# Optimization experiments

Measured on AMD Instinct MI355X. Metric: run time of the kernel, lower is better.

The kernel has to match this reference:

```python
import jax, jax.numpy as jnp
import numpy as np

IN_CH = 63      # positionally-encoded points
IN_VIEWS = 63   # positionally-encoded view dirs (must equal IN_CH per source bug)
UNITS = 256
N = 131072
SKIPS = (4,)


def _linear_init(key, fan_in, fan_out):
    # torch nn.Linear default: U(-1/sqrt(fan_in), 1/sqrt(fan_in)) for W and b
    kw, kb = jax.random.split(key)
    bound = 1.0 / np.sqrt(fan_in)
    W = jax.random.uniform(kw, (fan_in, fan_out), jnp.float32, -bound, bound)
    b = jax.random.uniform(kb, (fan_out,), jnp.float32, -bound, bound)
    return W, b


def setup_inputs() -> dict:
    key = jax.random.key(0)
    keys = jax.random.split(key, 16)
    inp = {}
    inp["x"] = jax.random.normal(keys[0], (N, IN_CH + IN_VIEWS), jnp.float32)
    # 8 backbone layers; layer idx 5 consumes skip-concat of width UNITS+IN_CH
    fan_ins = [IN_CH] + [UNITS + IN_CH if (i - 1) in SKIPS else UNITS for i in range(1, 8)]
    for i, fi in enumerate(fan_ins):
        W, b = _linear_init(keys[1 + i], fi, UNITS)
        inp[f"W{i}"], inp[f"b{i}"] = W, b
    inp["Wf"], inp["bf"] = _linear_init(keys[9], UNITS, UNITS)          # linear_feature
    inp["Wa"], inp["ba"] = _linear_init(keys[10], UNITS, 1)             # linear_alpha
    inp["Wv"], inp["bv"] = _linear_init(keys[11], IN_CH + UNITS, UNITS // 2)  # linear_views[0]
    inp["Wr"], inp["br"] = _linear_init(keys[12], UNITS // 2, 3)        # linear_rgb
    return inp


def reference(x, W0, b0, W1, b1, W2, b2, W3, b3, W4, b4, W5, b5, W6, b6, W7, b7,
              Wf, bf, Wa, ba, Wv, bv, Wr, br):
    pts = x[..., :IN_CH]
    views = x[..., IN_CH:]
    Ws = (W0, W1, W2, W3, W4, W5, W6, W7)
    bs = (b0, b1, b2, b3, b4, b5, b6, b7)
    h = pts
    for idx in range(8):
        h = jax.nn.relu(h @ Ws[idx] + bs[idx])
        if idx in SKIPS:
            h = jnp.concatenate([pts, h], axis=-1)  # [N, IN_CH + UNITS]
    alpha = h @ Wa + ba                       # [N, 1]
    feature = h @ Wf + bf                     # [N, UNITS]
    hv = jnp.concatenate([feature, views], axis=-1)   # [N, UNITS + IN_VIEWS]
    hv = jax.nn.relu(hv @ Wv + bv)            # [N, UNITS//2]
    rgb = hv @ Wr + br                        # [N, 3]
    return jnp.concatenate([rgb, alpha], axis=-1)     # [N, 4]
```

## Files before the change

kernel.cpp:

```cpp
#include <hip/hip_runtime.h>
#include <hip/hip_bf16.h>


typedef __bf16 bfrag __attribute__((ext_vector_type(8)));
typedef float  f4    __attribute__((ext_vector_type(4)));

constexpr int OFF_W0 = 0;
constexpr int OFF_W1 = 16384;
constexpr int OFF_W2 = 81920;
constexpr int OFF_W3 = 147456;
constexpr int OFF_W4 = 212992;
constexpr int OFF_W5 = 278528;
constexpr int OFF_W6 = 360448;
constexpr int OFF_W7 = 425984;
constexpr int OFF_WF = 491520;
constexpr int OFF_WV = 557056;
constexpr int OFF_WA = 598016;
constexpr int OFF_WR = 602112;
constexpr int WS_TOTAL = 604160;

__device__ __forceinline__ unsigned swz256(int row, int k) {
  return (unsigned)((row * 256 + k) ^ ((row & 7) << 3));
}
__device__ __forceinline__ unsigned swz64(int row, int k) {
  return (unsigned)((row * 64 + k) ^ ((row & 7) << 3));
}

template<int NCT, int NKS, int NCTS, int SSTR>
__device__ __forceinline__ void phase(f4 (&acc)[4][NCT],
    const unsigned short* __restrict__ src,
    const unsigned short* __restrict__ wt, int ks0, int ctb,
    int lane, int l15, int lk8) {
#pragma unroll
  for (int ks = 0; ks < NKS; ++ks) {
    const int kl = ks * 32 + lk8;
    bfrag a[4];
#pragma unroll
    for (int rt = 0; rt < 4; ++rt) {
      const unsigned idx = (SSTR == 256) ? swz256(rt * 16 + l15, kl)
                                         : swz64(rt * 16 + l15, kl);
      a[rt] = *(const bfrag*)(src + idx);
    }
    const unsigned short* wk =
        wt + ((size_t)(ks0 + ks) * NCTS + ctb) * 512 + lane * 8;
    constexpr int CH = (NCT < 2) ? NCT : 2;
#pragma unroll
    for (int c2 = 0; c2 < NCT; c2 += CH) {
      bfrag b[CH];
#pragma unroll
      for (int u = 0; u < CH; ++u)
        b[u] = *(const bfrag*)(wk + (size_t)(c2 + u) * 512);
#pragma unroll
      for (int u = 0; u < CH; ++u)
#pragma unroll
        for (int rt = 0; rt < 4; ++rt)
          acc[rt][c2 + u] = __builtin_amdgcn_mfma_f32_16x16x32_bf16(a[rt], b[u], acc[rt][c2 + u], 0, 0, 0);
    }
  }
}

template<int NCT>
__device__ __forceinline__ void init_acc(f4 (&acc)[4][NCT],
    const float* __restrict__ bias, int cb, int l15) {
#pragma unroll
  for (int ct = 0; ct < NCT; ++ct) {
    const float bv = bias[cb + ct * 16 + l15];
    f4 v = {bv, bv, bv, bv};
#pragma unroll
    for (int rt = 0; rt < 4; ++rt) acc[rt][ct] = v;
  }
}

template<bool RELU, int NCT>
__device__ __forceinline__ void store_h(f4 (&acc)[4][NCT],
    unsigned short* __restrict__ h, int cb, int l15, int lk4) {
#pragma unroll
  for (int ct = 0; ct < NCT; ++ct) {
    const int col = cb + ct * 16 + l15;
#pragma unroll
    for (int rt = 0; rt < 4; ++rt)
#pragma unroll
      for (int j = 0; j < 4; ++j) {
        float v = acc[rt][ct][j];
        if (RELU) v = fmaxf(v, 0.f);
        __bf16 bb = (__bf16)v;
        h[swz256(rt * 16 + lk4 + j, col)] = __builtin_bit_cast(unsigned short, bb);
      }
  }
}

__device__ __forceinline__ void stage_inputs(const float* __restrict__ x,
    unsigned short* pts, unsigned short* views, int rowg0, int tid) {
  const int row = tid >> 2, seg = tid & 3;
  const float* xr = x + (size_t)(rowg0 + row) * 126;
  bfrag v0, v1;
#pragma unroll
  for (int q = 0; q < 4; ++q) {
    const int c = seg * 16 + 2 * q;
    float2 t = *(const float2*)(xr + c);
    v0[2 * q]     = (c     < 63) ? (__bf16)t.x : (__bf16)0.f;
    v0[2 * q + 1] = (c + 1 < 63) ? (__bf16)t.y : (__bf16)0.f;
  }
#pragma unroll
  for (int q = 0; q < 4; ++q) {
    const int c = seg * 16 + 8 + 2 * q;
    float2 t = *(const float2*)(xr + c);
    v1[2 * q]     = (c     < 63) ? (__bf16)t.x : (__bf16)0.f;
    v1[2 * q + 1] = (c + 1 < 63) ? (__bf16)t.y : (__bf16)0.f;
  }
  *(bfrag*)(pts + swz64(row, seg * 16))     = v0;
  *(bfrag*)(pts + swz64(row, seg * 16 + 8)) = v1;
  bfrag w0, w1;
#pragma unroll
  for (int j = 0; j < 8; ++j) {
    const int c = seg * 16 + j;
    w0[j] = (c < 63) ? (__bf16)xr[63 + c] : (__bf16)0.f;
  }
#pragma unroll
  for (int j = 0; j < 8; ++j) {
    const int c = seg * 16 + 8 + j;
    w1[j] = (c < 63) ? (__bf16)xr[63 + c] : (__bf16)0.f;
  }
  *(bfrag*)(views + swz64(row, seg * 16))     = w0;
  *(bfrag*)(views + swz64(row, seg * 16 + 8)) = w1;
}

struct RepackArgs {
  const float *W0, *W1, *W2, *W3, *W4, *W5, *W6, *W7, *Wf, *Wv, *Wa, *Wr;
  unsigned short* ws;
};

__global__ void repack_kernel(RepackArgs a) {
  const int i = blockIdx.x * 256 + threadIdx.x;
  if (i >= WS_TOTAL) return;

  const float* src; int off, ncts, fanin, fanout; bool shift = false;
  int mode = 0;
  if      (i < OFF_W1) { src = a.W0; off = OFF_W0; ncts = 16; fanin = 63;  fanout = 256; }
  else if (i < OFF_W2) { src = a.W1; off = OFF_W1; ncts = 16; fanin = 256; fanout = 256; }
  else if (i < OFF_W3) { src = a.W2; off = OFF_W2; ncts = 16; fanin = 256; fanout = 256; }
  else if (i < OFF_W4) { src = a.W3; off = OFF_W3; ncts = 16; fanin = 256; fanout = 256; }
  else if (i < OFF_W5) { src = a.W4; off = OFF_W4; ncts = 16; fanin = 256; fanout = 256; }
  else if (i < OFF_W6) { src = a.W5; off = OFF_W5; ncts = 16; fanin = 319; fanout = 256; shift = true; }
  else if (i < OFF_W7) { src = a.W6; off = OFF_W6; ncts = 16; fanin = 256; fanout = 256; }
  else if (i < OFF_WF) { src = a.W7; off = OFF_W7; ncts = 16; fanin = 256; fanout = 256; }
  else if (i < OFF_WV) { src = a.Wf; off = OFF_WF; ncts = 16; fanin = 256; fanout = 256; }
  else if (i < OFF_WA) { src = a.Wv; off = OFF_WV; ncts = 8;  fanin = 319; fanout = 128; }
  else if (i < OFF_WR) { src = a.Wa; off = OFF_WA; ncts = 1;  fanin = 256; fanout = 1; mode = 1; }
  else                 { src = a.Wr; off = OFF_WR; ncts = 1;  fanin = 128; fanout = 3; mode = 2; }

  const int idx  = i - off;
  const int j    = idx & 7;
  const int lane = (idx >> 3) & 63;
  const int rem  = idx >> 9;
  const int ctg  = rem % ncts;
  const int ks   = rem / ncts;
  const int k    = ks * 32 + ((lane >> 4) << 3) + j;
  const int col  = ctg * 16 + (lane & 15);

  float v;
  if (mode == 1) {
    v = (col == 0 && k < fanin) ? src[k] : 0.f;
  } else if (mode == 2) {
    v = (col < 3 && k < fanin) ? src[(size_t)k * 3 + col] : 0.f;
  } else if (shift) {
    v = (k < 63) ? src[(size_t)k * 256 + col]
                 : ((k == 63) ? 0.f : src[(size_t)(k - 1) * 256 + col]);
  } else {
    v = (k < fanin) ? src[(size_t)k * fanout + col] : 0.f;
  }
  __bf16 bb = (__bf16)v;
  a.ws[i] = __builtin_bit_cast(unsigned short, bb);
}

struct MainArgs {
  const float* x;
  const unsigned short* ws;
  const float *b0, *b1, *b2, *b3, *b4, *b5, *b6, *b7;
  const float *bfc, *ba, *bv, *br;
  float* out;
};

__global__ __launch_bounds__(256, 2) void nerf_kernel(MainArgs A) {
  extern __shared__ unsigned short lds[];
  unsigned short* h     = lds;
  unsigned short* pts   = lds + 64 * 256;
  unsigned short* views = pts + 64 * 64;

  const int tid  = threadIdx.x;
  const int lane = tid & 63;
  const int wave = tid >> 6;
  const int l15 = lane & 15;
  const int lk8 = (lane >> 4) << 3;
  const int lk4 = (lane >> 4) << 2;
  const int cb  = wave * 64;
  const int ctb = wave * 4;
  const int rowg0 = blockIdx.x * 64;
  const unsigned short* ws = A.ws;

  stage_inputs(A.x, pts, views, rowg0, tid);
  __syncthreads();

  f4 acc[4][4];

  init_acc<4>(acc, A.b0, cb, l15);
  phase<4, 2, 16, 64>(acc, pts, ws + OFF_W0, 0, ctb, lane, l15, lk8);
  store_h<true, 4>(acc, h, cb, l15, lk4);
  __syncthreads();

  init_acc<4>(acc, A.b1, cb, l15);
  phase<4, 8, 16, 256>(acc, h, ws + OFF_W1, 0, ctb, lane, l15, lk8);
  __syncthreads();
  store_h<true, 4>(acc, h, cb, l15, lk4);
  __syncthreads();

  init_acc<4>(acc, A.b2, cb, l15);
  phase<4, 8, 16, 256>(acc, h, ws + OFF_W2, 0, ctb, lane, l15, lk8);
  __syncthreads();
  store_h<true, 4>(acc, h, cb, l15, lk4);
  __syncthreads();

  init_acc<4>(acc, A.b3, cb, l15);
  phase<4, 8, 16, 256>(acc, h, ws + OFF_W3, 0, ctb, lane, l15, lk8);
  __syncthreads();
  store_h<true, 4>(acc, h, cb, l15, lk4);
  __syncthreads();

  init_acc<4>(acc, A.b4, cb, l15);
  phase<4, 8, 16, 256>(acc, h, ws + OFF_W4, 0, ctb, lane, l15, lk8);
  __syncthreads();
  store_h<true, 4>(acc, h, cb, l15, lk4);
  __syncthreads();

  init_acc<4>(acc, A.b5, cb, l15);
  phase<4, 2, 16, 64>(acc, pts, ws + OFF_W5, 0, ctb, lane, l15, lk8);
  phase<4, 8, 16, 256>(acc, h, ws + OFF_W5, 2, ctb, lane, l15, lk8);
  __syncthreads();
  store_h<true, 4>(acc, h, cb, l15, lk4);
  __syncthreads();

  init_acc<4>(acc, A.b6, cb, l15);
  phase<4, 8, 16, 256>(acc, h, ws + OFF_W6, 0, ctb, lane, l15, lk8);
  __syncthreads();
  store_h<true, 4>(acc, h, cb, l15, lk4);
  __syncthreads();

  init_acc<4>(acc, A.b7, cb, l15);
  phase<4, 8, 16, 256>(acc, h, ws + OFF_W7, 0, ctb, lane, l15, lk8);
  __syncthreads();
  store_h<true, 4>(acc, h, cb, l15, lk4);
  __syncthreads();

  if (wave == 0) {
    f4 accA[4][1];
#pragma unroll
    for (int rt = 0; rt < 4; ++rt) accA[rt][0] = (f4){0.f, 0.f, 0.f, 0.f};
    phase<1, 8, 1, 256>(accA, h, ws + OFF_WA, 0, 0, lane, l15, lk8);
    if (l15 == 0) {
      const float ba0 = A.ba[0];
#pragma unroll
      for (int rt = 0; rt < 4; ++rt)
#pragma unroll
        for (int j = 0; j < 4; ++j)
          A.out[(size_t)(rowg0 + rt * 16 + lk4 + j) * 4 + 3] = accA[rt][0][j] + ba0;
    }
  }

  init_acc<4>(acc, A.bfc, cb, l15);
  phase<4, 8, 16, 256>(acc, h, ws + OFF_WF, 0, ctb, lane, l15, lk8);
  __syncthreads();
  store_h<false, 4>(acc, h, cb, l15, lk4);
  __syncthreads();

  {
    f4 acc2[4][2];
    const int cb2 = wave * 32;
    init_acc<2>(acc2, A.bv, cb2, l15);
    phase<2, 8, 8, 256>(acc2, h, ws + OFF_WV, 0, wave * 2, lane, l15, lk8);
    phase<2, 2, 8, 64>(acc2, views, ws + OFF_WV, 8, wave * 2, lane, l15, lk8);
    __syncthreads();
    store_h<true, 2>(acc2, h, cb2, l15, lk4);
  }
  __syncthreads();

  if (wave == 0) {
    f4 accR[4][1];
#pragma unroll
    for (int rt = 0; rt < 4; ++rt) accR[rt][0] = (f4){0.f, 0.f, 0.f, 0.f};
    phase<1, 4, 1, 256>(accR, h, ws + OFF_WR, 0, 0, lane, l15, lk8);
    if (l15 < 3) {
      const float bb = A.br[l15];
#pragma unroll
      for (int rt = 0; rt < 4; ++rt)
#pragma unroll
        for (int j = 0; j < 4; ++j)
          A.out[(size_t)(rowg0 + rt * 16 + lk4 + j) * 4 + l15] = accR[rt][0][j] + bb;
    }
  }
}

extern "C" void kernel_launch(void* const* d_in, const int* in_sizes, int n_in,
                              void* d_out, int out_size, void* d_ws, size_t ws_size,
                              hipStream_t stream) {
  RepackArgs ra;
  ra.W0 = (const float*)d_in[1];  ra.W1 = (const float*)d_in[3];
  ra.W2 = (const float*)d_in[5];  ra.W3 = (const float*)d_in[7];
  ra.W4 = (const float*)d_in[9];  ra.W5 = (const float*)d_in[11];
  ra.W6 = (const float*)d_in[13]; ra.W7 = (const float*)d_in[15];
  ra.Wf = (const float*)d_in[17]; ra.Wv = (const float*)d_in[21];
  ra.Wa = (const float*)d_in[19]; ra.Wr = (const float*)d_in[23];
  ra.ws = (unsigned short*)d_ws;
  repack_kernel<<<(WS_TOTAL + 255) / 256, 256, 0, stream>>>(ra);

  MainArgs ma;
  ma.x   = (const float*)d_in[0];
  ma.ws  = (const unsigned short*)d_ws;
  ma.b0  = (const float*)d_in[2];  ma.b1 = (const float*)d_in[4];
  ma.b2  = (const float*)d_in[6];  ma.b3 = (const float*)d_in[8];
  ma.b4  = (const float*)d_in[10]; ma.b5 = (const float*)d_in[12];
  ma.b6  = (const float*)d_in[14]; ma.b7 = (const float*)d_in[16];
  ma.bfc = (const float*)d_in[18];
  ma.ba  = (const float*)d_in[20];
  ma.bv  = (const float*)d_in[22];
  ma.br  = (const float*)d_in[24];
  ma.out = (float*)d_out;

  const int n    = in_sizes[0] / 126;
  const int grid = n / 64;

  hipFuncSetAttribute(reinterpret_cast<const void*>(nerf_kernel),
                      hipFuncAttributeMaxDynamicSharedMemorySize, 49152);
  nerf_kernel<<<grid, 256, 49152, stream>>>(ma);
}
```

Baseline: 176.6 us.

## Transpose MFMA operands to vectorize LDS stores, widen swizzle, raise occupancy

Swaps the A/B operands of the MFMA so each lane's accumulator holds four consecutive output columns of one row. The activation write-back to LDS then becomes a single packed 4-element store instead of four scattered 2-byte stores, and bias loads become float4. The LDS swizzle is widened to use the row modulo 32 to spread bank accesses for the new store pattern. The launch bounds are raised to three blocks per CU, which tightens the register budget and risks spills.

```diff
diff --git a/kernel.cpp b/kernel.cpp
--- a/kernel.cpp
+++ b/kernel.cpp
@@ -4,6 +4,7 @@
 
 typedef __bf16 bfrag __attribute__((ext_vector_type(8)));
 typedef float  f4    __attribute__((ext_vector_type(4)));
+typedef unsigned short us4 __attribute__((ext_vector_type(4)));
 
 constexpr int OFF_W0 = 0;
 constexpr int OFF_W1 = 16384;
@@ -20,7 +21,7 @@
 constexpr int WS_TOTAL = 604160;
 
 __device__ __forceinline__ unsigned swz256(int row, int k) {
-  return (unsigned)((row * 256 + k) ^ ((row & 7) << 3));
+  return (unsigned)((row * 256 + k) ^ ((row & 31) << 3));
 }
 __device__ __forceinline__ unsigned swz64(int row, int k) {
   return (unsigned)((row * 64 + k) ^ ((row & 7) << 3));
@@ -37,8 +38,8 @@
     bfrag a[4];
 #pragma unroll
     for (int rt = 0; rt < 4; ++rt) {
-      const unsigned idx = (SSTR == 256) ? swz256(rt * 16 + l15, kl)
-                                         : swz64(rt * 16 + l15, kl);
+      const int row = rt * 16 + l15;
+      const unsigned idx = (SSTR == 256) ? swz256(row, kl) : swz64(row, kl);
       a[rt] = *(const bfrag*)(src + idx);
     }
     const unsigned short* wk =
@@ -54,18 +55,18 @@
       for (int u = 0; u < CH; ++u)
 #pragma unroll
         for (int rt = 0; rt < 4; ++rt)
-          acc[rt][c2 + u] = __builtin_amdgcn_mfma_f32_16x16x32_bf16(a[rt], b[u], acc[rt][c2 + u], 0, 0, 0);
+          acc[rt][c2 + u] = __builtin_amdgcn_mfma_f32_16x16x32_bf16(b[u], a[rt], acc[rt][c2 + u], 0, 0, 0);
     }
   }
 }
 
 template<int NCT>
 __device__ __forceinline__ void init_acc(f4 (&acc)[4][NCT],
-    const float* __restrict__ bias, int cb, int l15) {
+    const float* __restrict__ bias, int cb, int lk4) {
 #pragma unroll
   for (int ct = 0; ct < NCT; ++ct) {
-    const float bv = bias[cb + ct * 16 + l15];
-    f4 v = {bv, bv, bv, bv};
+    const float4 bv = *(const float4*)(bias + cb + ct * 16 + lk4);
+    f4 v = {bv.x, bv.y, bv.z, bv.w};
 #pragma unroll
     for (int rt = 0; rt < 4; ++rt) acc[rt][ct] = v;
   }
@@ -76,16 +77,19 @@
     unsigned short* __restrict__ h, int cb, int l15, int lk4) {
 #pragma unroll
   for (int ct = 0; ct < NCT; ++ct) {
-    const int col = cb + ct * 16 + l15;
-#pragma unroll
-    for (int rt = 0; rt < 4; ++rt)
+    const int col0 = cb + ct * 16 + lk4;
+#pragma unroll
+    for (int rt = 0; rt < 4; ++rt) {
+      us4 packed;
 #pragma unroll
       for (int j = 0; j < 4; ++j) {
         float v = acc[rt][ct][j];
         if (RELU) v = fmaxf(v, 0.f);
         __bf16 bb = (__bf16)v;
-        h[swz256(rt * 16 + lk4 + j, col)] = __builtin_bit_cast(unsigned short, bb);
+        packed[j] = __builtin_bit_cast(unsigned short, bb);
       }
+      *(us4*)(h + swz256(rt * 16 + l15, col0)) = packed;
+    }
   }
 }
 
@@ -181,7 +185,7 @@
   float* out;
 };
 
-__global__ __launch_bounds__(256, 2) void nerf_kernel(MainArgs A) {
+__global__ __launch_bounds__(256, 3) void nerf_kernel(MainArgs A) {
   extern __shared__ unsigned short lds[];
   unsigned short* h     = lds;
   unsigned short* pts   = lds + 64 * 256;
@@ -203,49 +207,49 @@
 
   f4 acc[4][4];
 
-  init_acc<4>(acc, A.b0, cb, l15);
+  init_acc<4>(acc, A.b0, cb, lk4);
   phase<4, 2, 16, 64>(acc, pts, ws + OFF_W0, 0, ctb, lane, l15, lk8);
   store_h<true, 4>(acc, h, cb, l15, lk4);
   __syncthreads();
 
-  init_acc<4>(acc, A.b1, cb, l15);
+  init_acc<4>(acc, A.b1, cb, lk4);
   phase<4, 8, 16, 256>(acc, h, ws + OFF_W1, 0, ctb, lane, l15, lk8);
   __syncthreads();
   store_h<true, 4>(acc, h, cb, l15, lk4);
   __syncthreads();
 
-  init_acc<4>(acc, A.b2, cb, l15);
+  init_acc<4>(acc, A.b2, cb, lk4);
   phase<4, 8, 16, 256>(acc, h, ws + OFF_W2, 0, ctb, lane, l15, lk8);
   __syncthreads();
   store_h<true, 4>(acc, h, cb, l15, lk4);
   __syncthreads();
 
-  init_acc<4>(acc, A.b3, cb, l15);
+  init_acc<4>(acc, A.b3, cb, lk4);
   phase<4, 8, 16, 256>(acc, h, ws + OFF_W3, 0, ctb, lane, l15, lk8);
   __syncthreads();
   store_h<true, 4>(acc, h, cb, l15, lk4);
   __syncthreads();
 
-  init_acc<4>(acc, A.b4, cb, l15);
+  init_acc<4>(acc, A.b4, cb, lk4);
   phase<4, 8, 16, 256>(acc, h, ws + OFF_W4, 0, ctb, lane, l15, lk8);
   __syncthreads();
   store_h<true, 4>(acc, h, cb, l15, lk4);
   __syncthreads();
 
-  init_acc<4>(acc, A.b5, cb, l15);
+  init_acc<4>(acc, A.b5, cb, lk4);
   phase<4, 2, 16, 64>(acc, pts, ws + OFF_W5, 0, ctb, lane, l15, lk8);
   phase<4, 8, 16, 256>(acc, h, ws + OFF_W5, 2, ctb, lane, l15, lk8);
   __syncthreads();
   store_h<true, 4>(acc, h, cb, l15, lk4);
   __syncthreads();
 
-  init_acc<4>(acc, A.b6, cb, l15);
+  init_acc<4>(acc, A.b6, cb, lk4);
   phase<4, 8, 16, 256>(acc, h, ws + OFF_W6, 0, ctb, lane, l15, lk8);
   __syncthreads();
   store_h<true, 4>(acc, h, cb, l15, lk4);
   __syncthreads();
 
-  init_acc<4>(acc, A.b7, cb, l15);
+  init_acc<4>(acc, A.b7, cb, lk4);
   phase<4, 8, 16, 256>(acc, h, ws + OFF_W7, 0, ctb, lane, l15, lk8);
   __syncthreads();
   store_h<true, 4>(acc, h, cb, l15, lk4);
@@ -256,17 +260,15 @@
 #pragma unroll
     for (int rt = 0; rt < 4; ++rt) accA[rt][0] = (f4){0.f, 0.f, 0.f, 0.f};
     phase<1, 8, 1, 256>(accA, h, ws + OFF_WA, 0, 0, lane, l15, lk8);
-    if (l15 == 0) {
+    if (lk4 == 0) {
       const float ba0 = A.ba[0];
 #pragma unroll
       for (int rt = 0; rt < 4; ++rt)
-#pragma unroll
-        for (int j = 0; j < 4; ++j)
-          A.out[(size_t)(rowg0 + rt * 16 + lk4 + j) * 4 + 3] = accA[rt][0][j] + ba0;
-    }
-  }
-
-  init_acc<4>(acc, A.bfc, cb, l15);
+        A.out[(size_t)(rowg0 + rt * 16 + l15) * 4 + 3] = accA[rt][0][0] + ba0;
+    }
+  }
+
+  init_acc<4>(acc, A.bfc, cb, lk4);
   phase<4, 8, 16, 256>(acc, h, ws + OFF_WF, 0, ctb, lane, l15, lk8);
   __syncthreads();
   store_h<false, 4>(acc, h, cb, l15, lk4);
@@ -275,7 +277,7 @@
   {
     f4 acc2[4][2];
     const int cb2 = wave * 32;
-    init_acc<2>(acc2, A.bv, cb2, l15);
+    init_acc<2>(acc2, A.bv, cb2, lk4);
     phase<2, 8, 8, 256>(acc2, h, ws + OFF_WV, 0, wave * 2, lane, l15, lk8);
     phase<2, 2, 8, 64>(acc2, views, ws + OFF_WV, 8, wave * 2, lane, l15, lk8);
     __syncthreads();
@@ -288,13 +290,13 @@
 #pragma unroll
     for (int rt = 0; rt < 4; ++rt) accR[rt][0] = (f4){0.f, 0.f, 0.f, 0.f};
     phase<1, 4, 1, 256>(accR, h, ws + OFF_WR, 0, 0, lane, l15, lk8);
-    if (l15 < 3) {
-      const float bb = A.br[l15];
-#pragma unroll
-      for (int rt = 0; rt < 4; ++rt)
-#pragma unroll
-        for (int j = 0; j < 4; ++j)
-          A.out[(size_t)(rowg0 + rt * 16 + lk4 + j) * 4 + l15] = accR[rt][0][j] + bb;
+    if (lk4 == 0) {
+#pragma unroll
+      for (int rt = 0; rt < 4; ++rt) {
+        float* o = A.out + (size_t)(rowg0 + rt * 16 + l15) * 4;
+#pragma unroll
+        for (int j = 0; j < 3; ++j) o[j] = accR[rt][0][j] + A.br[j];
+      }
     }
   }
 }
```

Measured after the change: 252.7 us. 1.43x slower.
